# Kernel optimization log

Hardware: AMD Instinct MI355X
Metric: run time of the kernel (lower is better)

## Reference

```python
import jax, jax.numpy as jnp
import numpy as np

B, S, D, H = 2, 2048, 1024, 16
DK = D // H
SCALE = DK ** 0.5


def setup_inputs() -> dict:
    key = jax.random.key(0)
    ks = jax.random.split(key, 5)
    std = 1.0 / np.sqrt(D)
    return {
        "x": jax.random.normal(ks[0], (B, S, D), dtype=jnp.float32),
        "Wq": jax.random.normal(ks[1], (D, D), dtype=jnp.float32) * std,
        "Wk": jax.random.normal(ks[2], (D, D), dtype=jnp.float32) * std,
        "Wv": jax.random.normal(ks[3], (D, D), dtype=jnp.float32) * std,
        "Wo": jax.random.normal(ks[4], (D, D), dtype=jnp.float32) * std,
    }


def _split_heads(t):
    # [B, S, D] -> [B, H, S, DK]
    b, s, d = t.shape
    return t.reshape(b, s, H, DK).transpose(0, 2, 1, 3)


def reference(x, Wq, Wk, Wv, Wo):
    b, s, d = x.shape
    q = _split_heads(x @ Wq)
    k = _split_heads(x @ Wk)
    v = _split_heads(x @ Wv)
    # scores: [B, H, S, S]
    score = jnp.einsum("bhqd,bhkd->bhqk", q, k)
    causal = jnp.tril(jnp.ones((s, s), dtype=bool))[None, None]
    score = jnp.where(causal, score, -jnp.inf)
    attn = jax.nn.softmax(score / SCALE, axis=-1)
    out = jnp.einsum("bhqk,bhkd->bhqd", attn, v)
    out = out.transpose(0, 2, 1, 3).reshape(b, s, d)
    return out @ Wo
```

## Files before the change

### kernel.cpp

```cpp
#include <hip/hip_runtime.h>
#include <hip/hip_bf16.h>

typedef __bf16 bf16;
typedef __bf16 bf16x4 __attribute__((ext_vector_type(4)));
typedef __bf16 bf16x8 __attribute__((ext_vector_type(8)));
typedef float f32x4 __attribute__((ext_vector_type(4)));

#define MFMA16(a, b, c) __builtin_amdgcn_mfma_f32_16x16x32_bf16((a), (b), (c), 0, 0, 0)

__device__ __forceinline__ void async16(const void* g, void* l) {
  typedef const unsigned int __attribute__((address_space(1))) * GP;
  typedef unsigned int __attribute__((address_space(3))) * LP;
  __builtin_amdgcn_global_load_lds((GP)g, (LP)l, 16, 0, 0);
}

__global__ __launch_bounds__(256) void prep(
    const float* __restrict__ w0, const float* __restrict__ w1,
    const float* __restrict__ w2, const float* __restrict__ w3,
    const float* __restrict__ x, bf16* __restrict__ wtOut,
    bf16* __restrict__ xOut) {
  const int t = threadIdx.x;
  if (blockIdx.z == 4) {
    size_t base = ((size_t)(blockIdx.y * 16 + blockIdx.x)) * 16384;
#pragma unroll
    for (int p = 0; p < 16; ++p) {
      size_t i = base + (size_t)(p * 256 + t) * 4;
      f32x4 v = *(const f32x4*)&x[i];
      bf16 o[4];
#pragma unroll
      for (int j = 0; j < 4; ++j) o[j] = (bf16)v[j];
      *(ulong1*)&xOut[i] = *(ulong1*)o;
    }
    return;
  }
  __shared__ __align__(16) float tile[64][68];
  const float* src = (blockIdx.z == 0) ? w0 : (blockIdx.z == 1) ? w1
                   : (blockIdx.z == 2) ? w2 : w3;
  bf16* dst = wtOut + (size_t)blockIdx.z * (1024u * 1024u);
  const int bx = blockIdx.x, by = blockIdx.y;
#pragma unroll
  for (int p = 0; p < 4; ++p) {
    int idx = t + p * 256;
    int r = idx >> 4, c4 = idx & 15;
    *(f32x4*)&tile[r][c4 * 4] =
        *(const f32x4*)&src[(size_t)(by * 64 + r) * 1024 + bx * 64 + c4 * 4];
  }
  __syncthreads();
#pragma unroll
  for (int p = 0; p < 2; ++p) {
    int idx = t + p * 256;
    int rn = idx >> 3, c8 = idx & 7;
    bf16x8 v;
#pragma unroll
    for (int i = 0; i < 8; ++i) v[i] = (bf16)tile[c8 * 8 + i][rn];
    *(bf16x8*)&dst[(size_t)(bx * 64 + rn) * 1024 + by * 64 + c8 * 8] = v;
  }
}

template <typename OutT, int NI>
__global__ __launch_bounds__(256, 4) void gemm_bt(
    const bf16* __restrict__ A, const bf16* __restrict__ Bt,
    OutT* __restrict__ C, int btStrideZ, int cStrideZ, float scaleZ0,
    bf16* __restrict__ vtOut) {
  constexpr int XT = 1024 / (NI * 32);
  const int bid = blockIdx.x;
  const int rr = bid & 7, tt = bid >> 3;
  const int xb = tt % XT, yb = (tt / XT) * 8 + rr;
  const int zi = blockIdx.y;

  const int tid = threadIdx.x;
  const int wave = tid >> 6, lane = tid & 63;
  const int quad = lane >> 4, l16 = lane & 15;
  const int wm = wave >> 1, wn = wave & 1;
  const int m0 = yb * 128, n0 = xb * (NI * 32);
  const bf16* Bz = Bt + (size_t)zi * (size_t)btStrideZ;
  OutT* Cz = C + (size_t)zi * (size_t)cStrideZ;
  const float sc = (zi == 0) ? scaleZ0 : 1.0f;

  __shared__ __align__(16) bf16 lsA[2][128 * 32];
  __shared__ __align__(16) bf16 lsB[2][NI * 32 * 32];

  const int lrow = lane >> 2;
  const int cgX = (lane & 3) ^ ((lrow >> 1) & 3);
  const int fR = (l16 >> 1) & 3;

  f32x4 acc[4][NI];
#pragma unroll
  for (int i = 0; i < 4; ++i)
#pragma unroll
    for (int j = 0; j < NI; ++j) acc[i][j] = (f32x4){0.f, 0.f, 0.f, 0.f};

#pragma unroll
  for (int c = 0; c < 2; ++c) {
    int chunk = wave * 2 + c;
    int row = chunk * 16 + lrow;
    async16(&A[(size_t)(m0 + row) * 1024 + cgX * 8], &lsA[0][chunk * 512]);
  }
#pragma unroll
  for (int c = 0; c < NI / 2; ++c) {
    int chunk = wave * (NI / 2) + c;
    int row = chunk * 16 + lrow;
    async16(&Bz[(size_t)(n0 + row) * 1024 + cgX * 8], &lsB[0][chunk * 512]);
  }
  __syncthreads();

  for (int it = 0; it < 32; ++it) {
    const int cur = it & 1;
    if (it < 31) {
      int k0n = (it + 1) * 32;
#pragma unroll
      for (int c = 0; c < 2; ++c) {
        int chunk = wave * 2 + c;
        int row = chunk * 16 + lrow;
        async16(&A[(size_t)(m0 + row) * 1024 + k0n + cgX * 8],
                &lsA[cur ^ 1][chunk * 512]);
      }
#pragma unroll
      for (int c = 0; c < NI / 2; ++c) {
        int chunk = wave * (NI / 2) + c;
        int row = chunk * 16 + lrow;
        async16(&Bz[(size_t)(n0 + row) * 1024 + k0n + cgX * 8],
                &lsB[cur ^ 1][chunk * 512]);
      }
    }

    bf16x8 af[4], bfr[NI];
#pragma unroll
    for (int i = 0; i < 4; ++i) {
      int ra = wm * 64 + i * 16 + l16;
      af[i] = *(const bf16x8*)&lsA[cur][ra * 32 + ((quad ^ fR) * 8)];
    }
#pragma unroll
    for (int ni = 0; ni < NI; ++ni) {
      int rb = wn * (NI * 16) + ni * 16 + l16;
      bfr[ni] = *(const bf16x8*)&lsB[cur][rb * 32 + ((quad ^ fR) * 8)];
    }
#pragma unroll
    for (int mi = 0; mi < 4; ++mi)
#pragma unroll
      for (int ni = 0; ni < NI; ++ni)
        acc[mi][ni] = MFMA16(af[mi], bfr[ni], acc[mi][ni]);

    __syncthreads();
  }

  if (zi == 2 && vtOut != nullptr) {
#pragma unroll
    for (int mi = 0; mi < 4; ++mi)
#pragma unroll
      for (int ni = 0; ni < NI; ++ni) {
        int col = n0 + wn * (NI * 16) + ni * 16 + l16;
        int hd = col >> 6, d = col & 63;
        int row = m0 + wm * 64 + mi * 16 + quad * 4;
        int b = row >> 11, s = row & 2047;
        int s32 = s & 31;
        int sp = (s & ~31) + ((s32 & 12) << 1) + ((s32 >> 4) << 2);
        bf16 o[4];
#pragma unroll
        for (int r = 0; r < 4; ++r) o[r] = (bf16)acc[mi][ni][r];
        *(ulong1*)&vtOut[((size_t)(b * 16 + hd) * 64 + d) * 2048 + sp] =
            *(ulong1*)o;
      }
  } else {
#pragma unroll
    for (int mi = 0; mi < 4; ++mi)
#pragma unroll
      for (int ni = 0; ni < NI; ++ni) {
        int col = n0 + wn * (NI * 16) + ni * 16 + l16;
#pragma unroll
        for (int r = 0; r < 4; ++r) {
          int row = m0 + wm * 64 + mi * 16 + quad * 4 + r;
          Cz[(size_t)row * 1024 + col] = (OutT)(acc[mi][ni][r] * sc);
        }
      }
  }
}

__global__ __launch_bounds__(512, 4) void attn_fwd(
    const bf16* __restrict__ Q, const bf16* __restrict__ K,
    const bf16* __restrict__ Vt, bf16* __restrict__ O) {
  const int bid = blockIdx.x;
  const int xcd = bid & 7;
  const int idx = bid >> 3;
  const int rnd = idx >> 5;
  const int s   = idx & 31;
  const int bh  = xcd * 4 + (s & 3);
  const int x   = s >> 2;
  const int qt  = rnd ? (15 - x) : x;
  const int h = bh & 15, b = bh >> 4;
  const int tid = threadIdx.x;
  const int wave = tid >> 6, lane = tid & 63;
  const int quad = lane >> 4, l16 = lane & 15;

  __shared__ __align__(16) bf16 SMEM[32768];
  bf16* Qs = &SMEM[16384];

  const size_t base = ((size_t)b * 2048) * 1024 + (size_t)h * 64;
  const bf16* Qb = Q + base;
  const bf16* Kb = K + base;
  const bf16* Vtb = Vt + ((size_t)(b * 16 + h)) * 64 * 2048;
  bf16* Ob = O + base;

  const int lrow = lane >> 3;
  const int cgX = (lane & 7) ^ lrow;

#pragma unroll
  for (int c = 0; c < 2; ++c) {
    int chunk = wave * 2 + c;
    int row = chunk * 8 + lrow;
    async16(&Qb[(size_t)(qt * 128 + row) * 1024 + cgX * 8], &Qs[chunk * 512]);
  }
  {
    int row = wave * 8 + lrow;
    async16(&Kb[(size_t)row * 1024 + cgX * 8], &SMEM[0 * 8192 + wave * 512]);
    async16(&Vtb[(size_t)row * 2048 + cgX * 8],
            &SMEM[0 * 8192 + 4096 + wave * 512]);
    async16(&Kb[(size_t)(64 + row) * 1024 + cgX * 8],
            &SMEM[1 * 8192 + wave * 512]);
    async16(&Vtb[(size_t)row * 2048 + 64 + cgX * 8],
            &SMEM[1 * 8192 + 4096 + wave * 512]);
  }
  __syncthreads();

  bf16x8 aq[2];
#pragma unroll
  for (int ks = 0; ks < 2; ++ks) {
    int row = wave * 16 + l16;
    aq[ks] = *(const bf16x8*)&Qs[row * 64 + (((ks * 4 + quad) ^ (l16 & 7)) * 8)];
  }
  __syncthreads();

  const float NEG_INF = -__builtin_inff();
  f32x4 lsv = (f32x4){0.f, 0.f, 0.f, 0.f};
  f32x4 Oacc[4];
#pragma unroll
  for (int nt = 0; nt < 4; ++nt) Oacc[nt] = (f32x4){0.f, 0.f, 0.f, 0.f};

  const int kt_end = 2 * qt + 1;
  const int ktd = 2 * qt + (wave >> 2);

  for (int ktp = 0; ktp <= kt_end; ktp += 2) {
    {
      int row = wave * 8 + lrow;
      if (ktp + 2 <= kt_end) {
        int s2 = (ktp + 2) & 3;
        async16(&Kb[(size_t)((ktp + 2) * 64 + row) * 1024 + cgX * 8],
                &SMEM[s2 * 8192 + wave * 512]);
        async16(&Vtb[(size_t)row * 2048 + (ktp + 2) * 64 + cgX * 8],
                &SMEM[s2 * 8192 + 4096 + wave * 512]);
      }
      if (ktp + 3 <= kt_end) {
        int s3 = (ktp + 3) & 3;
        async16(&Kb[(size_t)((ktp + 3) * 64 + row) * 1024 + cgX * 8],
                &SMEM[s3 * 8192 + wave * 512]);
        async16(&Vtb[(size_t)row * 2048 + (ktp + 3) * 64 + cgX * 8],
                &SMEM[s3 * 8192 + 4096 + wave * 512]);
      }
    }

#pragma unroll
    for (int sub = 0; sub < 2; ++sub) {
      const int kt = ktp + sub;
      const int ko = (kt & 3) * 8192;
      const int vo = ko + 4096;
      if (kt <= ktd) {
        f32x4 sv[4];
#pragma unroll
        for (int nt = 0; nt < 4; ++nt) {
          int row = nt * 16 + l16;
          bf16x8 bk0 = *(const bf16x8*)&SMEM[ko + row * 64 +
                                             ((quad ^ (l16 & 7)) * 8)];
          bf16x8 bk1 = *(const bf16x8*)&SMEM[ko + row * 64 +
                                             (((4 + quad) ^ (l16 & 7)) * 8)];
          sv[nt] = (f32x4){0.f, 0.f, 0.f, 0.f};
          __builtin_amdgcn_s_setprio(1);
          sv[nt] = MFMA16(bk0, aq[0], sv[nt]);
          sv[nt] = MFMA16(bk1, aq[1], sv[nt]);
          __builtin_amdgcn_s_setprio(0);
        }

        if (kt == ktd) {
          const int q_rel = wave * 16 + l16;
          const int cb = (kt - 2 * qt) * 64;
#pragma unroll
          for (int nt = 0; nt < 4; ++nt) {
            const int kb = cb + nt * 16 + quad * 4;
#pragma unroll
            for (int r = 0; r < 4; ++r)
              if (kb + r > q_rel) sv[nt][r] = NEG_INF;
          }
        }

#pragma unroll
        for (int nt = 0; nt < 4; ++nt) {
#pragma unroll
          for (int r = 0; r < 4; ++r) sv[nt][r] = exp2f(sv[nt][r]);
          lsv += sv[nt];
        }
        bf16x8 apf[2];
#pragma unroll
        for (int a = 0; a < 2; ++a) {
          bf16x4 c0 = __builtin_convertvector(sv[2 * a], bf16x4);
          bf16x4 c1 = __builtin_convertvector(sv[2 * a + 1], bf16x4);
#pragma unroll
          for (int i = 0; i < 4; ++i) {
            apf[a][i] = c0[i];
            apf[a][4 + i] = c1[i];
          }
        }

#pragma unroll
        for (int nt = 0; nt < 4; ++nt) {
          const int R = nt * 16 + l16;
          bf16x8 bvf0 = *(const bf16x8*)&SMEM[vo + R * 64 +
                                              (((0 + quad) ^ (l16 & 7)) * 8)];
          bf16x8 bvf1 = *(const bf16x8*)&SMEM[vo + R * 64 +
                                              (((4 + quad) ^ (l16 & 7)) * 8)];
          __builtin_amdgcn_s_setprio(1);
          Oacc[nt] = MFMA16(apf[0], bvf0, Oacc[nt]);
          Oacc[nt] = MFMA16(apf[1], bvf1, Oacc[nt]);
          __builtin_amdgcn_s_setprio(0);
        }
      }
    }

    __syncthreads();
  }

  float ls_acc = lsv[0] + lsv[1] + lsv[2] + lsv[3];
  ls_acc += __shfl_xor(ls_acc, 16, 64);
  ls_acc += __shfl_xor(ls_acc, 32, 64);
  float rl[4];
#pragma unroll
  for (int r = 0; r < 4; ++r) rl[r] = 1.f / __shfl(ls_acc, quad * 4 + r, 64);
#pragma unroll
  for (int nt = 0; nt < 4; ++nt)
#pragma unroll
    for (int r = 0; r < 4; ++r) {
      int row = qt * 128 + wave * 16 + quad * 4 + r;
      Ob[(size_t)row * 1024 + nt * 16 + l16] = (bf16)(Oacc[nt][r] * rl[r]);
    }
}

extern "C" void kernel_launch(void* const* d_in, const int* in_sizes, int n_in,
                              void* d_out, int out_size, void* d_ws,
                              size_t ws_size, hipStream_t stream) {
  (void)in_sizes; (void)n_in; (void)out_size; (void)ws_size;
  const float* x  = (const float*)d_in[0];
  const float* Wq = (const float*)d_in[1];
  const float* Wk = (const float*)d_in[2];
  const float* Wv = (const float*)d_in[3];
  const float* Wo = (const float*)d_in[4];
  float* out = (float*)d_out;

  bf16* ws = (bf16*)d_ws;
  const size_t WELEM = 1024u * 1024u;
  const size_t TELEM = 4096u * 1024u;
  bf16* wt  = ws;
  bf16* xbf = ws + 4 * WELEM;
  bf16* q   = xbf + TELEM;
  bf16* k   = q + TELEM;
  bf16* vt  = k + TELEM;
  bf16* ao  = vt + TELEM;

  const float QSCALE = 0.125f * 1.44269504088896340736f;

  prep<<<dim3(16, 16, 5), 256, 0, stream>>>(Wq, Wk, Wv, Wo, x, wt, xbf);
  gemm_bt<bf16, 4><<<dim3(256, 3), 256, 0, stream>>>(
      xbf, wt, q, (int)WELEM, (int)TELEM, QSCALE, vt);
  attn_fwd<<<dim3(512), 512, 0, stream>>>(q, k, vt, ao);
  gemm_bt<float, 2><<<dim3(512, 1), 256, 0, stream>>>(
      ao, wt + 3 * WELEM, out, 0, 0, 1.0f, nullptr);
}
```

Measured before the change: 169.1 us.

## Shrink attention query tile to 64 rows with 4-wave blocks and double buffering

Each attention block now handles 64 query rows with 256 threads instead of 128 rows with 512 threads. The grid doubles to 1024 blocks, and the block-to-tile mapping is reworked to interleave heavy and light causal tiles across XCDs. The K/V pipeline drops from a 4-stage, two-tiles-per-iteration scheme to a simple double buffer, which cuts LDS to 40 KB and removes the per-wave diagonal skip logic. exp2f is replaced with the hardware exp2 builtin. The aim is better load balance and occupancy, at the cost of more K/V reloads per query row and less prefetch depth.

```diff
diff --git a/kernel.cpp b/kernel.cpp
--- a/kernel.cpp
+++ b/kernel.cpp
@@ -176,23 +176,23 @@
   }
 }
 
-__global__ __launch_bounds__(512, 4) void attn_fwd(
+__global__ __launch_bounds__(256, 4) void attn_fwd(
     const bf16* __restrict__ Q, const bf16* __restrict__ K,
     const bf16* __restrict__ Vt, bf16* __restrict__ O) {
   const int bid = blockIdx.x;
   const int xcd = bid & 7;
-  const int idx = bid >> 3;
-  const int rnd = idx >> 5;
-  const int s   = idx & 31;
-  const int bh  = xcd * 4 + (s & 3);
-  const int x   = s >> 2;
-  const int qt  = rnd ? (15 - x) : x;
+  const int i = bid >> 3;
+  const int g = i & 3;
+  const int j = i >> 2;
+  const int a = j & 7, bq = j >> 3;
+  const int qt = (bq < 2) ? (31 - 2 * a - bq) : (2 * a + (bq & 1));
+  const int bh = xcd * 4 + g;
   const int h = bh & 15, b = bh >> 4;
   const int tid = threadIdx.x;
   const int wave = tid >> 6, lane = tid & 63;
   const int quad = lane >> 4, l16 = lane & 15;
 
-  __shared__ __align__(16) bf16 SMEM[32768];
+  __shared__ __align__(16) bf16 SMEM[20480];
   bf16* Qs = &SMEM[16384];
 
   const size_t base = ((size_t)b * 2048) * 1024 + (size_t)h * 64;
@@ -208,17 +208,9 @@
   for (int c = 0; c < 2; ++c) {
     int chunk = wave * 2 + c;
     int row = chunk * 8 + lrow;
-    async16(&Qb[(size_t)(qt * 128 + row) * 1024 + cgX * 8], &Qs[chunk * 512]);
-  }
-  {
-    int row = wave * 8 + lrow;
-    async16(&Kb[(size_t)row * 1024 + cgX * 8], &SMEM[0 * 8192 + wave * 512]);
-    async16(&Vtb[(size_t)row * 2048 + cgX * 8],
-            &SMEM[0 * 8192 + 4096 + wave * 512]);
-    async16(&Kb[(size_t)(64 + row) * 1024 + cgX * 8],
-            &SMEM[1 * 8192 + wave * 512]);
-    async16(&Vtb[(size_t)row * 2048 + 64 + cgX * 8],
-            &SMEM[1 * 8192 + 4096 + wave * 512]);
+    async16(&Qb[(size_t)(qt * 64 + row) * 1024 + cgX * 8], &Qs[chunk * 512]);
+    async16(&Kb[(size_t)row * 1024 + cgX * 8], &SMEM[chunk * 512]);
+    async16(&Vtb[(size_t)row * 2048 + cgX * 8], &SMEM[4096 + chunk * 512]);
   }
   __syncthreads();
 
@@ -228,7 +220,6 @@
     int row = wave * 16 + l16;
     aq[ks] = *(const bf16x8*)&Qs[row * 64 + (((ks * 4 + quad) ^ (l16 & 7)) * 8)];
   }
-  __syncthreads();
 
   const float NEG_INF = -__builtin_inff();
   f32x4 lsv = (f32x4){0.f, 0.f, 0.f, 0.f};
@@ -236,92 +227,79 @@
 #pragma unroll
   for (int nt = 0; nt < 4; ++nt) Oacc[nt] = (f32x4){0.f, 0.f, 0.f, 0.f};
 
-  const int kt_end = 2 * qt + 1;
-  const int ktd = 2 * qt + (wave >> 2);
-
-  for (int ktp = 0; ktp <= kt_end; ktp += 2) {
-    {
-      int row = wave * 8 + lrow;
-      if (ktp + 2 <= kt_end) {
-        int s2 = (ktp + 2) & 3;
-        async16(&Kb[(size_t)((ktp + 2) * 64 + row) * 1024 + cgX * 8],
-                &SMEM[s2 * 8192 + wave * 512]);
-        async16(&Vtb[(size_t)row * 2048 + (ktp + 2) * 64 + cgX * 8],
-                &SMEM[s2 * 8192 + 4096 + wave * 512]);
-      }
-      if (ktp + 3 <= kt_end) {
-        int s3 = (ktp + 3) & 3;
-        async16(&Kb[(size_t)((ktp + 3) * 64 + row) * 1024 + cgX * 8],
-                &SMEM[s3 * 8192 + wave * 512]);
-        async16(&Vtb[(size_t)row * 2048 + (ktp + 3) * 64 + cgX * 8],
-                &SMEM[s3 * 8192 + 4096 + wave * 512]);
-      }
-    }
-
-#pragma unroll
-    for (int sub = 0; sub < 2; ++sub) {
-      const int kt = ktp + sub;
-      const int ko = (kt & 3) * 8192;
-      const int vo = ko + 4096;
-      if (kt <= ktd) {
-        f32x4 sv[4];
-#pragma unroll
-        for (int nt = 0; nt < 4; ++nt) {
-          int row = nt * 16 + l16;
-          bf16x8 bk0 = *(const bf16x8*)&SMEM[ko + row * 64 +
-                                             ((quad ^ (l16 & 7)) * 8)];
-          bf16x8 bk1 = *(const bf16x8*)&SMEM[ko + row * 64 +
-                                             (((4 + quad) ^ (l16 & 7)) * 8)];
-          sv[nt] = (f32x4){0.f, 0.f, 0.f, 0.f};
-          __builtin_amdgcn_s_setprio(1);
-          sv[nt] = MFMA16(bk0, aq[0], sv[nt]);
-          sv[nt] = MFMA16(bk1, aq[1], sv[nt]);
-          __builtin_amdgcn_s_setprio(0);
-        }
-
-        if (kt == ktd) {
-          const int q_rel = wave * 16 + l16;
-          const int cb = (kt - 2 * qt) * 64;
-#pragma unroll
-          for (int nt = 0; nt < 4; ++nt) {
-            const int kb = cb + nt * 16 + quad * 4;
-#pragma unroll
-            for (int r = 0; r < 4; ++r)
-              if (kb + r > q_rel) sv[nt][r] = NEG_INF;
-          }
-        }
-
-#pragma unroll
-        for (int nt = 0; nt < 4; ++nt) {
-#pragma unroll
-          for (int r = 0; r < 4; ++r) sv[nt][r] = exp2f(sv[nt][r]);
-          lsv += sv[nt];
-        }
-        bf16x8 apf[2];
-#pragma unroll
-        for (int a = 0; a < 2; ++a) {
-          bf16x4 c0 = __builtin_convertvector(sv[2 * a], bf16x4);
-          bf16x4 c1 = __builtin_convertvector(sv[2 * a + 1], bf16x4);
-#pragma unroll
-          for (int i = 0; i < 4; ++i) {
-            apf[a][i] = c0[i];
-            apf[a][4 + i] = c1[i];
-          }
-        }
-
-#pragma unroll
-        for (int nt = 0; nt < 4; ++nt) {
-          const int R = nt * 16 + l16;
-          bf16x8 bvf0 = *(const bf16x8*)&SMEM[vo + R * 64 +
-                                              (((0 + quad) ^ (l16 & 7)) * 8)];
-          bf16x8 bvf1 = *(const bf16x8*)&SMEM[vo + R * 64 +
-                                              (((4 + quad) ^ (l16 & 7)) * 8)];
-          __builtin_amdgcn_s_setprio(1);
-          Oacc[nt] = MFMA16(apf[0], bvf0, Oacc[nt]);
-          Oacc[nt] = MFMA16(apf[1], bvf1, Oacc[nt]);
-          __builtin_amdgcn_s_setprio(0);
-        }
-      }
+  for (int kt = 0; kt <= qt; ++kt) {
+    const int cur = kt & 1;
+    if (kt < qt) {
+      const int ns = (cur ^ 1) * 8192;
+#pragma unroll
+      for (int c = 0; c < 2; ++c) {
+        int chunk = wave * 2 + c;
+        int row = chunk * 8 + lrow;
+        async16(&Kb[(size_t)((kt + 1) * 64 + row) * 1024 + cgX * 8],
+                &SMEM[ns + chunk * 512]);
+        async16(&Vtb[(size_t)row * 2048 + (kt + 1) * 64 + cgX * 8],
+                &SMEM[ns + 4096 + chunk * 512]);
+      }
+    }
+
+    const int ko = cur * 8192;
+    const int vo = ko + 4096;
+
+    f32x4 sv[4];
+#pragma unroll
+    for (int nt = 0; nt < 4; ++nt) {
+      int row = nt * 16 + l16;
+      bf16x8 bk0 =
+          *(const bf16x8*)&SMEM[ko + row * 64 + ((quad ^ (l16 & 7)) * 8)];
+      bf16x8 bk1 =
+          *(const bf16x8*)&SMEM[ko + row * 64 + (((4 + quad) ^ (l16 & 7)) * 8)];
+      sv[nt] = (f32x4){0.f, 0.f, 0.f, 0.f};
+      __builtin_amdgcn_s_setprio(1);
+      sv[nt] = MFMA16(bk0, aq[0], sv[nt]);
+      sv[nt] = MFMA16(bk1, aq[1], sv[nt]);
+      __builtin_amdgcn_s_setprio(0);
+    }
+
+    if (kt == qt) {
+      const int q_rel = wave * 16 + l16;
+#pragma unroll
+      for (int nt = 0; nt < 4; ++nt) {
+        const int kb = nt * 16 + quad * 4;
+#pragma unroll
+        for (int r = 0; r < 4; ++r)
+          if (kb + r > q_rel) sv[nt][r] = NEG_INF;
+      }
+    }
+
+#pragma unroll
+    for (int nt = 0; nt < 4; ++nt) {
+#pragma unroll
+      for (int r = 0; r < 4; ++r) sv[nt][r] = __builtin_amdgcn_exp2f(sv[nt][r]);
+      lsv += sv[nt];
+    }
+    bf16x8 apf[2];
+#pragma unroll
+    for (int a2 = 0; a2 < 2; ++a2) {
+      bf16x4 c0 = __builtin_convertvector(sv[2 * a2], bf16x4);
+      bf16x4 c1 = __builtin_convertvector(sv[2 * a2 + 1], bf16x4);
+#pragma unroll
+      for (int i2 = 0; i2 < 4; ++i2) {
+        apf[a2][i2] = c0[i2];
+        apf[a2][4 + i2] = c1[i2];
+      }
+    }
+
+#pragma unroll
+    for (int nt = 0; nt < 4; ++nt) {
+      const int R = nt * 16 + l16;
+      bf16x8 bvf0 =
+          *(const bf16x8*)&SMEM[vo + R * 64 + ((quad ^ (l16 & 7)) * 8)];
+      bf16x8 bvf1 =
+          *(const bf16x8*)&SMEM[vo + R * 64 + (((4 + quad) ^ (l16 & 7)) * 8)];
+      __builtin_amdgcn_s_setprio(1);
+      Oacc[nt] = MFMA16(apf[0], bvf0, Oacc[nt]);
+      Oacc[nt] = MFMA16(apf[1], bvf1, Oacc[nt]);
+      __builtin_amdgcn_s_setprio(0);
     }
 
     __syncthreads();
@@ -337,7 +315,7 @@
   for (int nt = 0; nt < 4; ++nt)
 #pragma unroll
     for (int r = 0; r < 4; ++r) {
-      int row = qt * 128 + wave * 16 + quad * 4 + r;
+      int row = qt * 64 + wave * 16 + quad * 4 + r;
       Ob[(size_t)row * 1024 + nt * 16 + l16] = (bf16)(Oacc[nt][r] * rl[r]);
     }
 }
@@ -368,7 +346,7 @@
   prep<<<dim3(16, 16, 5), 256, 0, stream>>>(Wq, Wk, Wv, Wo, x, wt, xbf);
   gemm_bt<bf16, 4><<<dim3(256, 3), 256, 0, stream>>>(
       xbf, wt, q, (int)WELEM, (int)TELEM, QSCALE, vt);
-  attn_fwd<<<dim3(512), 512, 0, stream>>>(q, k, vt, ao);
+  attn_fwd<<<dim3(1024), 256, 0, stream>>>(q, k, vt, ao);
   gemm_bt<float, 2><<<dim3(512, 1), 256, 0, stream>>>(
       ao, wt + 3 * WELEM, out, 0, 0, 1.0f, nullptr);
 }
```

Result: faster. 159.9 us (-5.4%).
